# Performance work log

Hardware: AMD Instinct MI355X
Metric: run time of the kernel (lower is better)

Reference implementation:

```python
import jax, jax.numpy as jnp
import numpy as np

N = 50000   # num nodes (learners)
M = 1000    # num scenes (columns of init)
D = 256     # embedding_dim
E = 800000  # edges per meta-path graph


def _glorot(k, shape):
    fan = float(sum(shape)) if len(shape) > 1 else float(shape[0])
    return jax.random.normal(k, shape, dtype=jnp.float32) * (2.0 / fan) ** 0.5


def setup_inputs() -> dict:
    key = jax.random.key(0)
    ks = jax.random.split(key, 16)
    inp = {
        'init': jax.random.uniform(ks[0], (N, M), dtype=jnp.float32),
        'edge_index_scs': jax.random.randint(ks[1], (2, E), 0, N, dtype=jnp.int32),
        'edge_attr_scs': jax.random.uniform(ks[2], (E,), dtype=jnp.float32),
        'edge_index_sls': jax.random.randint(ks[3], (2, E), 0, N, dtype=jnp.int32),
        'edge_attr_sls': jax.random.uniform(ks[4], (E,), dtype=jnp.float32),
        'proj_w1': _glorot(ks[5], (1, 16)),
        'proj_b1': jnp.zeros((16,), jnp.float32),
        'proj_w2': _glorot(ks[6], (16, D)),
        'proj_b2': jnp.zeros((D,), jnp.float32),
    }
    for j, name in enumerate(['scs', 'sls']):
        for l in range(3):
            inp[f'{name}_W{l+1}'] = _glorot(ks[7 + j * 3 + l], (D, D))
            inp[f'{name}_b{l+1}'] = jnp.zeros((D,), jnp.float32)
    inp['att_w'] = _glorot(ks[13], (D,))
    inp['att_b'] = jnp.zeros((), jnp.float32)
    return inp


def _gcn_layer(x, row, col, w, W, b):
    xl = x @ W                                                  # [N, D]
    deg = jax.ops.segment_sum(w, col, num_segments=N) + 1.0     # self-loop weight 1
    dinv = jax.lax.rsqrt(deg)
    norm = dinv[row] * w * dinv[col]                            # [E]
    agg = jax.ops.segment_sum(norm[:, None] * xl[row], col, num_segments=N)
    return agg + (dinv * dinv)[:, None] * xl + b                # self-loop term


def _gcn3(x, ei, ea, W1, b1, W2, b2, W3, b3):
    row, col = ei[0], ei[1]
    h = jax.nn.relu(_gcn_layer(x, row, col, ea, W1, b1))
    h = jax.nn.relu(_gcn_layer(h, row, col, ea, W2, b2))
    return jax.nn.relu(_gcn_layer(h, row, col, ea, W3, b3))


def _projection(init, w1, b1, w2, b2):
    # torch loop: per row, MLP over float nonzero *indices*, mean-pooled.
    # Embedding only depends on the column index -> precompute per-column embs.
    cols = jnp.arange(M, dtype=jnp.float32)[:, None]            # [M, 1]
    col_emb = jax.nn.relu(cols @ w1 + b1) @ w2 + b2             # [M, D]
    mask = (init != 0).astype(jnp.float32)                      # [N, M]
    cnt = mask.sum(axis=1)                                      # [N]
    emb = (mask @ col_emb) / jnp.maximum(cnt, 1.0)[:, None]
    return jnp.where((cnt > 0)[:, None], emb, 0.0)


def reference(init, edge_index_scs, edge_attr_scs, edge_index_sls, edge_attr_sls,
              proj_w1, proj_b1, proj_w2, proj_b2,
              scs_W1, scs_b1, scs_W2, scs_b2, scs_W3, scs_b3,
              sls_W1, sls_b1, sls_W2, sls_b2, sls_W3, sls_b3,
              att_w, att_b):
    emb0 = _projection(init, proj_w1, proj_b1, proj_w2, proj_b2)
    out_scs = _gcn3(emb0, edge_index_scs, edge_attr_scs, scs_W1, scs_b1, scs_W2, scs_b2, scs_W3, scs_b3)
    out_sls = _gcn3(emb0, edge_index_sls, edge_attr_sls, sls_W1, sls_b1, sls_W2, sls_b2, sls_W3, sls_b3)
    emb = jnp.stack([out_scs, out_sls], axis=0)                 # [2, N, D]
    scores = jnp.einsum('pnd,d->pn', emb, att_w) + att_b        # [2, N]
    attw = jax.nn.softmax(scores, axis=0)                       # softmax over paths
    return jnp.einsum('pn,pnd->nd', attw, emb)                  # [N, D]
```

## Files before the change

kernel.cpp:

```cpp
#include <hip/hip_runtime.h>

#define N_NODES 50000
#define M_SCENE 1000
#define DIM 256
#define N_EDGES 800000
#define CAP 64
#define NBUCK 196
#define NPAD (NBUCK * 256)
#define BCAP 5120
#define ECHUNK 4096
#define SMAX 64
#define QBM 64
#define QBK 64
#define QTILES 782

typedef __attribute__((ext_vector_type(8))) short short8;
typedef __attribute__((ext_vector_type(8))) unsigned short ushort8v;
typedef __attribute__((ext_vector_type(4))) float floatx4;

__device__ __forceinline__ float bf2f(unsigned short u) {
    union { unsigned int i; float f; } v; v.i = ((unsigned int)u) << 16; return v.f;
}
__device__ __forceinline__ unsigned short f2bf(float f) {
    union { float f; unsigned int i; } v; v.f = f;
    unsigned int r = (v.i + 0x7FFFu + ((v.i >> 16) & 1u)) >> 16;
    return (unsigned short)r;
}

__device__ __forceinline__ int pinv(int k) {
    return (k & ~63) + ((k & 15) << 2) + ((k >> 4) & 3);
}

__global__ void k_col_emb(const float* __restrict__ w1, const float* __restrict__ b1,
                          const float* __restrict__ w2, const float* __restrict__ b2,
                          float* __restrict__ col_emb) {
    int m = blockIdx.x;
    int d = threadIdx.x;
    float acc = b2[d];
#pragma unroll
    for (int h = 0; h < 16; ++h) {
        float r = fmaf((float)m, w1[h], b1[h]);
        r = fmaxf(r, 0.f);
        acc = fmaf(r, w2[h * DIM + d], acc);
    }
    col_emb[m * DIM + d] = acc;
}

__global__ void k_setup(const float* __restrict__ col_emb, float* __restrict__ colsum,
                        unsigned short* __restrict__ vbf, int* __restrict__ bfill,
                        int* __restrict__ nspec) {
    int d = threadIdx.x;
    float s = 0.f;
    for (int m = 0; m < M_SCENE; ++m) s += col_emb[m * DIM + d];
    colsum[d] = s;
    vbf[d] = f2bf(s * (1.0f / (float)M_SCENE));
    for (int i = d; i < 2 * NBUCK; i += 256) bfill[i] = 0;
    if (d == 0) *nspec = 0;
}

__global__ __launch_bounds__(256) void k_scan(const float* __restrict__ init,
                                              int* __restrict__ nspec,
                                              int* __restrict__ spec_rows) {
    int row = blockIdx.x * 4 + (threadIdx.x >> 6);
    if (row >= N_NODES) return;
    int lane = threadIdx.x & 63;
    const float4* r4 = (const float4*)(init + (size_t)row * M_SCENE);
    bool z = false;
    for (int i = lane; i < 250; i += 64) {
        float4 v = r4[i];
        z |= (v.x == 0.f) | (v.y == 0.f) | (v.z == 0.f) | (v.w == 0.f);
    }
    unsigned long long mb = __ballot(z);
    if (lane == 0 && mb) {
        int p = atomicAdd(nspec, 1);
        if (p < SMAX) spec_rows[p] = row;
    }
}

__global__ __launch_bounds__(256) void k_spec(const float* __restrict__ init,
                                              const float* __restrict__ col_emb,
                                              const float* __restrict__ colsum,
                                              const int* __restrict__ nspec,
                                              const int* __restrict__ spec_rows,
                                              float* __restrict__ spec_emb) {
    int j = blockIdx.x;
    int ns = *nspec; if (ns > SMAX) ns = SMAX;
    if (j >= ns) return;
    int n = spec_rows[j];
    int t = threadIdx.x;
    __shared__ int zlist[SMAX];
    __shared__ int zcnt;
    if (t == 0) zcnt = 0;
    __syncthreads();
    const float4* row4 = (const float4*)(init + (size_t)n * M_SCENE);
    if (t < 250) {
        float4 v = row4[t];
        if (v.x == 0.f) { int p = atomicAdd(&zcnt, 1); if (p < SMAX) zlist[p] = 4 * t; }
        if (v.y == 0.f) { int p = atomicAdd(&zcnt, 1); if (p < SMAX) zlist[p] = 4 * t + 1; }
        if (v.z == 0.f) { int p = atomicAdd(&zcnt, 1); if (p < SMAX) zlist[p] = 4 * t + 2; }
        if (v.w == 0.f) { int p = atomicAdd(&zcnt, 1); if (p < SMAX) zlist[p] = 4 * t + 3; }
    }
    __syncthreads();
    int zc = zcnt; if (zc > SMAX) zc = SMAX;
    int nz = M_SCENE - zcnt;
    float s = colsum[t];
    for (int i = 0; i < zc; ++i) s -= col_emb[zlist[i] * DIM + t];
    float e = (nz > 0) ? (s / (float)nz) : 0.f;
    spec_emb[j * DIM + t] = bf2f(f2bf(e));
}

__global__ __launch_bounds__(256) void k_delta(const float* __restrict__ spec_emb,
                                               const unsigned short* __restrict__ vbf,
                                               const unsigned short* __restrict__ Wt,
                                               const int* __restrict__ nspec,
                                               float* __restrict__ delta) {
    int j = blockIdx.x, g = blockIdx.y;
    int ns = *nspec; if (ns > SMAX) ns = SMAX;
    if (j < SMAX && j >= ns) return;
    int d = threadIdx.x;
    const unsigned short* W = Wt + (size_t)(g * 3 + 0) * DIM * DIM + (size_t)d * DIM;
    float acc = 0.f;
    if (j == SMAX) {
        for (int k = 0; k < DIM; ++k) acc = fmaf(bf2f(vbf[k]), bf2f(W[k]), acc);
    } else {
        const float* x = spec_emb + j * DIM;
        for (int k = 0; k < DIM; ++k) acc = fmaf(x[k], bf2f(W[k]), acc);
    }
    delta[((size_t)g * (SMAX + 1) + j) * DIM + d] = acc;
}

__global__ __launch_bounds__(256) void k_prep_w(const float* W0, const float* W1, const float* W2,
                                                const float* W3, const float* W4, const float* W5,
                                                unsigned short* __restrict__ Wt) {
    const float* Ws[6] = {W0, W1, W2, W3, W4, W5};
    int L = blockIdx.z;
    const float* W = Ws[L];
    unsigned short* T = Wt + (size_t)L * DIM * DIM;
    bool perm = (L % 3) != 0;
    __shared__ float tile[32][33];
    int k0 = blockIdx.y * 32, n0 = blockIdx.x * 32;
    int tx = threadIdx.x & 31, ty = threadIdx.x >> 5;
    for (int r = ty; r < 32; r += 8) tile[r][tx] = W[(k0 + r) * DIM + n0 + tx];
    __syncthreads();
    int k = k0 + tx;
    int p = perm ? pinv(k) : k;
    for (int r = ty; r < 32; r += 8) T[(size_t)(n0 + r) * DIM + p] = f2bf(tile[tx][r]);
}

__global__ __launch_bounds__(256) void k_bucket(const int* __restrict__ ei0,
                                                const float* __restrict__ ea0,
                                                const int* __restrict__ ei1,
                                                const float* __restrict__ ea1,
                                                int* __restrict__ bfill,
                                                unsigned long long* __restrict__ bdata) {
    int g = blockIdx.y;
    const int* ei = g ? ei1 : ei0;
    const float* ea = g ? ea1 : ea0;
    __shared__ int hist[NBUCK];
    __shared__ int base[NBUCK];
    int t = threadIdx.x;
    for (int i = t; i < NBUCK; i += 256) hist[i] = 0;
    __syncthreads();
    int e0 = blockIdx.x * ECHUNK;
#pragma unroll
    for (int k = 0; k < ECHUNK / 256; ++k) {
        int e = e0 + k * 256 + t;
        if (e < N_EDGES) atomicAdd(&hist[ei[N_EDGES + e] >> 8], 1);
    }
    __syncthreads();
    for (int i = t; i < NBUCK; i += 256) {
        int h = hist[i];
        base[i] = h ? atomicAdd(&bfill[g * NBUCK + i], h) : 0;
        hist[i] = 0;
    }
    __syncthreads();
#pragma unroll
    for (int k = 0; k < ECHUNK / 256; ++k) {
        int e = e0 + k * 256 + t;
        if (e < N_EDGES) {
            int r = ei[e], c = ei[N_EDGES + e];
            float a = ea[e];
            int b = c >> 8;
            int off = atomicAdd(&hist[b], 1) + base[b];
            if (off < BCAP)
                bdata[((size_t)g * NBUCK + b) * BCAP + off] =
                    ((unsigned long long)(c & 255) << 32) |
                    ((unsigned long long)((unsigned int)r << 16) | f2bf(a));
        }
    }
}

__global__ __launch_bounds__(256) void k_csr(const int* __restrict__ bfill,
                                             const unsigned long long* __restrict__ bdata,
                                             int* __restrict__ cnt,
                                             unsigned int* __restrict__ slots,
                                             float* __restrict__ dinv) {
    int g = blockIdx.y, b = blockIdx.x;
    int t = threadIdx.x;
    __shared__ unsigned int lslots[256 * CAP];
    __shared__ int lcnt[256];
    lcnt[t] = 0;
    __syncthreads();
    int n = bfill[g * NBUCK + b]; if (n > BCAP) n = BCAP;
    const unsigned long long* src = bdata + ((size_t)g * NBUCK + b) * BCAP;
    for (int i = t; i < n; i += 256) {
        unsigned long long p = src[i];
        int lc = (int)(p >> 32);
        int pos = atomicAdd(&lcnt[lc], 1);
        if (pos < CAP) lslots[lc * CAP + pos] = (unsigned int)p;
    }
    __syncthreads();
    int node = b * 256 + t;
    if (node < N_NODES) {
        int c = lcnt[t]; if (c > CAP) c = CAP;
        cnt[g * N_NODES + node] = c;
        float a = 0.f;
        for (int i = 0; i < c; ++i)
            a += bf2f((unsigned short)(lslots[t * CAP + i] & 0xFFFFu));
        dinv[g * N_NODES + node] = rsqrtf(1.0f + a);
    }
    unsigned int* dst = slots + ((size_t)g * NPAD + b * 256) * CAP;
    for (int i = t; i < 256 * CAP; i += 256) dst[i] = lslots[i];
}

__global__ __launch_bounds__(256) void k_layer1(const float* __restrict__ dinv,
                                                const int* __restrict__ cnt,
                                                const unsigned int* __restrict__ slots,
                                                const int* __restrict__ nspec_p,
                                                const int* __restrict__ spec_rows,
                                                const float* __restrict__ delta,
                                                const float* __restrict__ bias0,
                                                const float* __restrict__ bias1,
                                                unsigned short* __restrict__ outp) {
    int ng = blockIdx.x * 4 + (threadIdx.x >> 6);
    if (ng >= 2 * N_NODES) return;
    int lane = threadIdx.x & 63;
    int g = ng >= N_NODES;
    int gbase = g ? N_NODES : 0;
    int n = ng - gbase;
    const float* bias = g ? bias1 : bias0;
    int c = cnt[ng];
    float dn = dinv[ng];
    int ns = *nspec_p; if (ns > SMAX) ns = SMAX;
    size_t sbase = ((size_t)g * NPAD + n) * CAP;
    float w = 0.f;
    int match = -1;
    if (lane < c) {
        unsigned int sl = slots[sbase + lane];
        int s = (int)(sl >> 16);
        w = dinv[gbase + s] * bf2f((unsigned short)(sl & 0xFFFFu)) * dn;
        for (int k = 0; k < ns; ++k)
            if (spec_rows[k] == s) { match = k; break; }
    }
    float alpha = w;
#pragma unroll
    for (int off = 32; off; off >>= 1) alpha += __shfl_xor(alpha, off, 64);
    alpha += dn * dn;
    int pc0 = ((lane >> 4) << 6) + (lane & 15);
    const float* dbase = delta + (size_t)g * (SMAX + 1) * DIM;
    const float* vwp = dbase + SMAX * DIM;
    float vw0 = vwp[pc0], vw1 = vwp[pc0 + 16], vw2 = vwp[pc0 + 32], vw3 = vwp[pc0 + 48];
    float c0 = 0.f, c1 = 0.f, c2 = 0.f, c3 = 0.f;
    unsigned long long mb = __ballot(match >= 0);
    while (mb) {
        int l = __ffsll((unsigned long long)mb) - 1;
        mb &= mb - 1;
        float wj = __shfl(w, l, 64);
        int mj = __shfl(match, l, 64);
        const float* D = dbase + mj * DIM;
        c0 = fmaf(wj, D[pc0] - vw0, c0);
        c1 = fmaf(wj, D[pc0 + 16] - vw1, c1);
        c2 = fmaf(wj, D[pc0 + 32] - vw2, c2);
        c3 = fmaf(wj, D[pc0 + 48] - vw3, c3);
    }
    int selfm = -1;
    for (int k = 0; k < ns; ++k) if (spec_rows[k] == n) selfm = k;
    if (selfm >= 0) {
        float sw = dn * dn;
        const float* D = dbase + selfm * DIM;
        c0 = fmaf(sw, D[pc0] - vw0, c0);
        c1 = fmaf(sw, D[pc0 + 16] - vw1, c1);
        c2 = fmaf(sw, D[pc0 + 32] - vw2, c2);
        c3 = fmaf(sw, D[pc0 + 48] - vw3, c3);
    }
    ushort4 o;
    o.x = f2bf(fmaxf(fmaf(alpha, vw0, c0) + bias[pc0], 0.f));
    o.y = f2bf(fmaxf(fmaf(alpha, vw1, c1) + bias[pc0 + 16], 0.f));
    o.z = f2bf(fmaxf(fmaf(alpha, vw2, c2) + bias[pc0 + 32], 0.f));
    o.w = f2bf(fmaxf(fmaf(alpha, vw3, c3) + bias[pc0 + 48], 0.f));
    ((ushort4*)outp)[(size_t)ng * 64 + lane] = o;
}

__global__ __launch_bounds__(256) void k_gemm_q(const unsigned short* __restrict__ X0,
                                                const unsigned short* __restrict__ X1,
                                                const unsigned short* __restrict__ W0,
                                                const unsigned short* __restrict__ W1,
                                                unsigned int* __restrict__ xq,
                                                float* __restrict__ qscale) {
    __shared__ unsigned short As[2][QBM * QBK];
    __shared__ unsigned short Bs[2][DIM * QBK];
    int tid = threadIdx.x;
    int w = tid >> 6, l = tid & 63;
    int gb = blockIdx.x >= QTILES;
    int bx = blockIdx.x - (gb ? QTILES : 0);
    const unsigned short* Xb = gb ? X1 : X0;
    const unsigned short* Wt = gb ? W1 : W0;
    int row0 = bx * QBM;
    floatx4 acc[16] = {};

    int innerA = (tid & 7) * 16;
    const unsigned short* gA[2];
    int soffA[2];
#pragma unroll
    for (int i = 0; i < 2; ++i) {
        int r = i * 32 + (tid >> 3);
        int grow = row0 + r; if (grow >= N_NODES) grow = N_NODES - 1;
        gA[i] = Xb + (size_t)grow * DIM + (innerA >> 1);
        soffA[i] = r * 128 + (innerA ^ ((r & 7) << 4));
    }
    const unsigned short* gB[8];
    int soffB[8];
#pragma unroll
    for (int i = 0; i < 8; ++i) {
        int nr = i * 32 + (tid >> 3);
        gB[i] = Wt + (size_t)nr * DIM + (innerA >> 1);
        soffB[i] = nr * 128 + (innerA ^ ((nr & 7) << 4));
    }
    ushort8v pa[2], pb[8];
#pragma unroll
    for (int i = 0; i < 2; ++i) pa[i] = *(const ushort8v*)(gA[i]);
#pragma unroll
    for (int i = 0; i < 8; ++i) pb[i] = *(const ushort8v*)(gB[i]);
#pragma unroll
    for (int i = 0; i < 2; ++i) *(ushort8v*)((char*)As[0] + soffA[i]) = pa[i];
#pragma unroll
    for (int i = 0; i < 8; ++i) *(ushort8v*)((char*)Bs[0] + soffB[i]) = pb[i];
    __syncthreads();

    int cur = 0;
#pragma unroll
    for (int kt = 0; kt < DIM / QBK; ++kt) {
        if (kt < DIM / QBK - 1) {
            int koff = (kt + 1) * QBK;
#pragma unroll
            for (int i = 0; i < 2; ++i) pa[i] = *(const ushort8v*)(gA[i] + koff);
#pragma unroll
            for (int i = 0; i < 8; ++i) pb[i] = *(const ushort8v*)(gB[i] + koff);
        }
#pragma unroll
        for (int s = 0; s < 2; ++s) {
            int kb = s * 64 + (l >> 4) * 16;
            int r = w * 16 + (l & 15);
            short8 a = *(const short8*)((const char*)As[cur] + r * 128 + (kb ^ ((r & 7) << 4)));
#pragma unroll
            for (int nn = 0; nn < 16; ++nn) {
                int nr = nn * 16 + (l & 15);
                short8 b = *(const short8*)((const char*)Bs[cur] + nr * 128 + (kb ^ ((nr & 7) << 4)));
                acc[nn] = __builtin_amdgcn_mfma_f32_16x16x32_bf16(a, b, acc[nn], 0, 0, 0);
            }
        }
        if (kt < DIM / QBK - 1) {
#pragma unroll
            for (int i = 0; i < 2; ++i) *(ushort8v*)((char*)As[cur ^ 1] + soffA[i]) = pa[i];
#pragma unroll
            for (int i = 0; i < 8; ++i) *(ushort8v*)((char*)Bs[cur ^ 1] + soffB[i]) = pb[i];
            __syncthreads();
            cur ^= 1;
        }
    }
    int c = l & 15, g4 = l >> 4;
    float inv[4], sc[4];
#pragma unroll
    for (int j = 0; j < 4; ++j) {
        float m = 0.f;
#pragma unroll
        for (int nn = 0; nn < 16; ++nn) m = fmaxf(m, fabsf(acc[nn][j]));
#pragma unroll
        for (int off = 1; off < 16; off <<= 1) m = fmaxf(m, __shfl_xor(m, off, 64));
        inv[j] = (m > 0.f) ? (127.0f / m) : 0.f;
        sc[j] = m * (1.0f / 127.0f);
    }
    int rbase = row0 + w * 16 + g4 * 4;
    int gofs = gb ? N_NODES : 0;
#pragma unroll
    for (int j = 0; j < 4; ++j) {
        int grow = rbase + j;
        if (grow < N_NODES) {
            if (c == 0) qscale[gofs + grow] = sc[j];
#pragma unroll
            for (int t = 0; t < 4; ++t) {
                unsigned int q0 = (unsigned int)(int)rintf(fmaf(acc[4 * t + 0][j], inv[j], 128.f));
                unsigned int q1 = (unsigned int)(int)rintf(fmaf(acc[4 * t + 1][j], inv[j], 128.f));
                unsigned int q2 = (unsigned int)(int)rintf(fmaf(acc[4 * t + 2][j], inv[j], 128.f));
                unsigned int q3 = (unsigned int)(int)rintf(fmaf(acc[4 * t + 3][j], inv[j], 128.f));
                xq[((size_t)(gofs + grow)) * 64 + t * 16 + c] =
                    q0 | (q1 << 8) | (q2 << 16) | (q3 << 24);
            }
        }
    }
}

__device__ __forceinline__ float ub(unsigned int u, int k) {
    return (float)((u >> (8 * k)) & 0xFFu);
}

__global__ __launch_bounds__(256) void k_aggregate(const unsigned int* __restrict__ xq,
                                                   const float* __restrict__ scale,
                                                   const float* __restrict__ dinv,
                                                   const int* __restrict__ cnt,
                                                   const unsigned int* __restrict__ slots,
                                                   const float* __restrict__ bias0,
                                                   const float* __restrict__ bias1,
                                                   unsigned short* __restrict__ out) {
    int ng = blockIdx.x * 4 + (threadIdx.x >> 6);
    if (ng >= 2 * N_NODES) return;
    int lane = threadIdx.x & 63;
    int g = ng >= N_NODES;
    int gbase = g ? N_NODES : 0;
    const float* bias = g ? bias1 : bias0;
    int c = cnt[ng];
    float dn = dinv[ng];
    size_t sbase = ((size_t)g * NPAD + (ng - gbase)) * CAP;
    unsigned int packed = 0;
    float wdr = 0.f;
    if (lane < c) {
        unsigned int sl = slots[sbase + lane];
        int s = (int)(sl >> 16);
        float w = dinv[gbase + s] * bf2f((unsigned short)(sl & 0xFFFFu)) * dn;
        unsigned short h = f2bf(w * scale[gbase + s]);
        packed = (sl & 0xFFFF0000u) | (unsigned int)h;
        wdr = bf2f(h);
    }
    float wdsum = wdr;
#pragma unroll
    for (int off = 32; off; off >>= 1) wdsum += __shfl_xor(wdsum, off, 64);
    size_t gb64 = (size_t)gbase * 64;
    float a0 = 0.f, a1 = 0.f, a2 = 0.f, a3 = 0.f;
    int j = 0;
    for (; j + 7 < c; j += 8) {
        unsigned int v[8];
        float wq[8];
#pragma unroll
        for (int q = 0; q < 8; ++q) {
            unsigned int u = __shfl(packed, j + q, 64);
            wq[q] = bf2f((unsigned short)(u & 0xFFFFu));
            v[q] = xq[gb64 + (size_t)(u >> 16) * 64 + lane];
        }
#pragma unroll
        for (int q = 0; q < 8; ++q) {
            a0 = fmaf(wq[q], ub(v[q], 0), a0); a1 = fmaf(wq[q], ub(v[q], 1), a1);
            a2 = fmaf(wq[q], ub(v[q], 2), a2); a3 = fmaf(wq[q], ub(v[q], 3), a3);
        }
    }
    for (; j < c; ++j) {
        unsigned int u = __shfl(packed, j, 64);
        float w0 = bf2f((unsigned short)(u & 0xFFFFu));
        unsigned int v0 = xq[gb64 + (size_t)(u >> 16) * 64 + lane];
        a0 = fmaf(w0, ub(v0, 0), a0); a1 = fmaf(w0, ub(v0, 1), a1);
        a2 = fmaf(w0, ub(v0, 2), a2); a3 = fmaf(w0, ub(v0, 3), a3);
    }
    float sd = dn * dn * scale[ng];
    unsigned int us = xq[(size_t)ng * 64 + lane];
    a0 = fmaf(sd, ub(us, 0), a0); a1 = fmaf(sd, ub(us, 1), a1);
    a2 = fmaf(sd, ub(us, 2), a2); a3 = fmaf(sd, ub(us, 3), a3);
    float off128 = 128.f * (wdsum + sd);
    int pc0 = ((lane >> 4) << 6) + (lane & 15);
    ushort4 o;
    o.x = f2bf(fmaxf(a0 - off128 + bias[pc0], 0.f));
    o.y = f2bf(fmaxf(a1 - off128 + bias[pc0 + 16], 0.f));
    o.z = f2bf(fmaxf(a2 - off128 + bias[pc0 + 32], 0.f));
    o.w = f2bf(fmaxf(a3 - off128 + bias[pc0 + 48], 0.f));
    ((ushort4*)out)[(size_t)ng * 64 + lane] = o;
}

__global__ __launch_bounds__(256) void k_agg_combine(const unsigned int* __restrict__ xq,
                                                     const float* __restrict__ scale,
                                                     const float* __restrict__ dinv,
                                                     const int* __restrict__ cnt,
                                                     const unsigned int* __restrict__ slots,
                                                     const float* __restrict__ bias0,
                                                     const float* __restrict__ bias1,
                                                     const float* __restrict__ att_w,
                                                     const float* __restrict__ att_b,
                                                     float* __restrict__ out) {
    int n = blockIdx.x * 4 + (threadIdx.x >> 6);
    if (n >= N_NODES) return;
    int lane = threadIdx.x & 63;
    int c0 = cnt[n];
    int c1 = cnt[N_NODES + n];
    float dn0 = dinv[n], dn1 = dinv[N_NODES + n];
    unsigned int p0 = 0, p1 = 0;
    float wr0 = 0.f, wr1 = 0.f;
    if (lane < c0) {
        unsigned int sl = slots[(size_t)n * CAP + lane];
        int s = (int)(sl >> 16);
        float w = dinv[s] * bf2f((unsigned short)(sl & 0xFFFFu)) * dn0;
        unsigned short h = f2bf(w * scale[s]);
        p0 = (sl & 0xFFFF0000u) | (unsigned int)h;
        wr0 = bf2f(h);
    }
    if (lane < c1) {
        unsigned int sl = slots[((size_t)NPAD + n) * CAP + lane];
        int s = (int)(sl >> 16);
        float w = dinv[N_NODES + s] * bf2f((unsigned short)(sl & 0xFFFFu)) * dn1;
        unsigned short h = f2bf(w * scale[N_NODES + s]);
        p1 = (sl & 0xFFFF0000u) | (unsigned int)h;
        wr1 = bf2f(h);
    }
    float ws0 = wr0, ws1 = wr1;
#pragma unroll
    for (int off = 32; off; off >>= 1) {
        ws0 += __shfl_xor(ws0, off, 64);
        ws1 += __shfl_xor(ws1, off, 64);
    }
    size_t g1 = (size_t)N_NODES * 64;
    float A0 = 0.f, A1 = 0.f, A2 = 0.f, A3 = 0.f;
    float B0 = 0.f, B1 = 0.f, B2 = 0.f, B3 = 0.f;
    int j = 0;
    for (; j + 7 < c0; j += 8) {
        unsigned int v[8]; float wq[8];
#pragma unroll
        for (int q = 0; q < 8; ++q) {
            unsigned int u = __shfl(p0, j + q, 64);
            wq[q] = bf2f((unsigned short)(u & 0xFFFFu));
            v[q] = xq[(size_t)(u >> 16) * 64 + lane];
        }
#pragma unroll
        for (int q = 0; q < 8; ++q) {
            A0 = fmaf(wq[q], ub(v[q], 0), A0); A1 = fmaf(wq[q], ub(v[q], 1), A1);
            A2 = fmaf(wq[q], ub(v[q], 2), A2); A3 = fmaf(wq[q], ub(v[q], 3), A3);
        }
    }
    for (; j < c0; ++j) {
        unsigned int u = __shfl(p0, j, 64);
        float w0 = bf2f((unsigned short)(u & 0xFFFFu));
        unsigned int v0 = xq[(size_t)(u >> 16) * 64 + lane];
        A0 = fmaf(w0, ub(v0, 0), A0); A1 = fmaf(w0, ub(v0, 1), A1);
        A2 = fmaf(w0, ub(v0, 2), A2); A3 = fmaf(w0, ub(v0, 3), A3);
    }
    j = 0;
    for (; j + 7 < c1; j += 8) {
        unsigned int v[8]; float wq[8];
#pragma unroll
        for (int q = 0; q < 8; ++q) {
            unsigned int u = __shfl(p1, j + q, 64);
            wq[q] = bf2f((unsigned short)(u & 0xFFFFu));
            v[q] = xq[g1 + (size_t)(u >> 16) * 64 + lane];
        }
#pragma unroll
        for (int q = 0; q < 8; ++q) {
            B0 = fmaf(wq[q], ub(v[q], 0), B0); B1 = fmaf(wq[q], ub(v[q], 1), B1);
            B2 = fmaf(wq[q], ub(v[q], 2), B2); B3 = fmaf(wq[q], ub(v[q], 3), B3);
        }
    }
    for (; j < c1; ++j) {
        unsigned int u = __shfl(p1, j, 64);
        float w0 = bf2f((unsigned short)(u & 0xFFFFu));
        unsigned int v0 = xq[g1 + (size_t)(u >> 16) * 64 + lane];
        B0 = fmaf(w0, ub(v0, 0), B0); B1 = fmaf(w0, ub(v0, 1), B1);
        B2 = fmaf(w0, ub(v0, 2), B2); B3 = fmaf(w0, ub(v0, 3), B3);
    }
    float sd0 = dn0 * dn0 * scale[n];
    float sd1 = dn1 * dn1 * scale[N_NODES + n];
    unsigned int us0 = xq[(size_t)n * 64 + lane];
    unsigned int us1 = xq[g1 + (size_t)n * 64 + lane];
    A0 = fmaf(sd0, ub(us0, 0), A0); A1 = fmaf(sd0, ub(us0, 1), A1);
    A2 = fmaf(sd0, ub(us0, 2), A2); A3 = fmaf(sd0, ub(us0, 3), A3);
    B0 = fmaf(sd1, ub(us1, 0), B0); B1 = fmaf(sd1, ub(us1, 1), B1);
    B2 = fmaf(sd1, ub(us1, 2), B2); B3 = fmaf(sd1, ub(us1, 3), B3);
    float offA = 128.f * (ws0 + sd0);
    float offB = 128.f * (ws1 + sd1);
    int pc0 = ((lane >> 4) << 6) + (lane & 15);
    float va0 = fmaxf(A0 - offA + bias0[pc0], 0.f);
    float va1 = fmaxf(A1 - offA + bias0[pc0 + 16], 0.f);
    float va2 = fmaxf(A2 - offA + bias0[pc0 + 32], 0.f);
    float va3 = fmaxf(A3 - offA + bias0[pc0 + 48], 0.f);
    float vb0 = fmaxf(B0 - offB + bias1[pc0], 0.f);
    float vb1 = fmaxf(B1 - offB + bias1[pc0 + 16], 0.f);
    float vb2 = fmaxf(B2 - offB + bias1[pc0 + 32], 0.f);
    float vb3 = fmaxf(B3 - offB + bias1[pc0 + 48], 0.f);
    float pa = va0 * att_w[pc0] + va1 * att_w[pc0 + 16]
             + va2 * att_w[pc0 + 32] + va3 * att_w[pc0 + 48];
    float pb = vb0 * att_w[pc0] + vb1 * att_w[pc0 + 16]
             + vb2 * att_w[pc0 + 32] + vb3 * att_w[pc0 + 48];
#pragma unroll
    for (int off = 32; off > 0; off >>= 1) {
        pa += __shfl_xor(pa, off, 64);
        pb += __shfl_xor(pb, off, 64);
    }
    float bbias = att_b[0];
    float sa = pa + bbias, sb = pb + bbias;
    float mx = fmaxf(sa, sb);
    float ea = __expf(sa - mx), eb = __expf(sb - mx);
    float inv = 1.f / (ea + eb);
    float wa = ea * inv, wb = eb * inv;
    float* orow = out + (size_t)n * DIM;
    orow[pc0]      = wa * va0 + wb * vb0;
    orow[pc0 + 16] = wa * va1 + wb * vb1;
    orow[pc0 + 32] = wa * va2 + wb * vb2;
    orow[pc0 + 48] = wa * va3 + wb * vb3;
}

static inline size_t align256(size_t x) { return (x + 255) & ~(size_t)255; }

extern "C" void kernel_launch(void* const* d_in, const int* in_sizes, int n_in,
                              void* d_out, int out_size, void* d_ws, size_t ws_size,
                              hipStream_t stream) {
    const float* init  = (const float*)d_in[0];
    const int*   ei0 = (const int*)d_in[1];
    const float* ea0 = (const float*)d_in[2];
    const int*   ei1 = (const int*)d_in[3];
    const float* ea1 = (const float*)d_in[4];
    const float* pw1 = (const float*)d_in[5];
    const float* pb1 = (const float*)d_in[6];
    const float* pw2 = (const float*)d_in[7];
    const float* pb2 = (const float*)d_in[8];
    const float* W[2][3];
    const float* B[2][3];
    for (int g = 0; g < 2; ++g)
        for (int l = 0; l < 3; ++l) {
            W[g][l] = (const float*)d_in[9 + g * 6 + l * 2];
            B[g][l] = (const float*)d_in[9 + g * 6 + l * 2 + 1];
        }
    const float* att_w = (const float*)d_in[21];
    const float* att_b = (const float*)d_in[22];
    float* out = (float*)d_out;

    char* ws = (char*)d_ws;
    size_t NBH  = (size_t)N_NODES * DIM * sizeof(unsigned short);
    size_t NBH2 = 2 * NBH;
    unsigned short* ACTa  = (unsigned short*)ws; ws += align256(NBH2);
    unsigned short* ACTb  = (unsigned short*)ws; ws += align256(NBH2);
    unsigned int*   XQ    = (unsigned int*)ws;   ws += align256((size_t)2 * N_NODES * DIM);
    float* qscale = (float*)ws; ws += align256((size_t)2 * N_NODES * 4);
    unsigned short* Wt    = (unsigned short*)ws; ws += align256((size_t)6 * DIM * DIM * 2);
    float* colemb = (float*)ws; ws += align256((size_t)M_SCENE * DIM * 4);
    float* colsum = (float*)ws; ws += align256(DIM * 4);
    unsigned short* vbf = (unsigned short*)ws; ws += align256(DIM * 2);
    int*   nspec  = (int*)ws;   ws += align256(4);
    int*   specr  = (int*)ws;   ws += align256(SMAX * 4);
    float* specemb = (float*)ws; ws += align256((size_t)SMAX * DIM * 4);
    float* delta  = (float*)ws; ws += align256((size_t)2 * (SMAX + 1) * DIM * 4);
    float* dinv   = (float*)ws; ws += align256((size_t)2 * N_NODES * 4);
    int*   cnt    = (int*)ws;   ws += align256((size_t)2 * N_NODES * 4);
    int*   bfill  = (int*)ws;   ws += align256((size_t)2 * NBUCK * 4);
    unsigned long long* bdata = (unsigned long long*)ws;
    ws += align256((size_t)2 * NBUCK * BCAP * 8);
    unsigned int* slots = (unsigned int*)ws; ws += align256((size_t)2 * NPAD * CAP * 4);

    dim3 b256(256);
    k_prep_w<<<dim3(8, 8, 6), b256, 0, stream>>>(W[0][0], W[0][1], W[0][2],
                                                 W[1][0], W[1][1], W[1][2], Wt);
    k_col_emb<<<M_SCENE, b256, 0, stream>>>(pw1, pb1, pw2, pb2, colemb);
    k_setup<<<1, b256, 0, stream>>>(colemb, colsum, vbf, bfill, nspec);
    k_scan<<<(N_NODES + 3) / 4, b256, 0, stream>>>(init, nspec, specr);
    k_spec<<<SMAX, b256, 0, stream>>>(init, colemb, colsum, nspec, specr, specemb);
    k_delta<<<dim3(SMAX + 1, 2), b256, 0, stream>>>(specemb, vbf, Wt, nspec, delta);

    k_bucket<<<dim3((N_EDGES + ECHUNK - 1) / ECHUNK, 2), b256, 0, stream>>>(
        ei0, ea0, ei1, ea1, bfill, bdata);
    k_csr<<<dim3(NBUCK, 2), b256, 0, stream>>>(bfill, bdata, cnt, slots, dinv);

    int nblkAgg = (2 * N_NODES + 3) / 4;
    k_layer1<<<nblkAgg, b256, 0, stream>>>(dinv, cnt, slots, nspec, specr, delta,
                                           B[0][0], B[1][0], ACTa);
    k_gemm_q<<<2 * QTILES, b256, 0, stream>>>(ACTa, ACTa + (size_t)N_NODES * DIM,
                                              Wt + (size_t)1 * DIM * DIM,
                                              Wt + (size_t)4 * DIM * DIM, XQ, qscale);
    k_aggregate<<<nblkAgg, b256, 0, stream>>>(XQ, qscale, dinv, cnt, slots,
                                              B[0][1], B[1][1], ACTb);
    k_gemm_q<<<2 * QTILES, b256, 0, stream>>>(ACTb, ACTb + (size_t)N_NODES * DIM,
                                              Wt + (size_t)2 * DIM * DIM,
                                              Wt + (size_t)5 * DIM * DIM, XQ, qscale);
    k_agg_combine<<<(N_NODES + 3) / 4, b256, 0, stream>>>(
        XQ, qscale, dinv, cnt, slots, B[0][2], B[1][2], att_w, att_b, out);
}
```

Measured before the change: 405.6 us.

## Merge row scan with edge bucketing and fuse spec/delta kernels

Combines the zero-row scan of init and the edge bucketing pass into one launch, using a block-index range split so the two independent workloads run concurrently. It also fuses the special-row embedding computation with the first-layer delta GEMV, keeping the row in shared memory and covering both paths in one block instead of two. This drops two kernel launches and a global intermediate buffer. In exchange the combined kernel reserves bucket shared memory even for scan blocks, and each delta block now does both paths serially.

Result: faster. 393.6 us (-3.0%).

```diff
diff --git a/kernel.cpp b/kernel.cpp
--- a/kernel.cpp
+++ b/kernel.cpp
@@ -9,6 +9,7 @@
 #define NPAD (NBUCK * 256)
 #define BCAP 5120
 #define ECHUNK 4096
+#define EBBLK 196
 #define SMAX 64
 #define QBM 64
 #define QBK 64
@@ -58,12 +59,54 @@
     if (d == 0) *nspec = 0;
 }
 
-__global__ __launch_bounds__(256) void k_scan(const float* __restrict__ init,
-                                              int* __restrict__ nspec,
-                                              int* __restrict__ spec_rows) {
-    int row = blockIdx.x * 4 + (threadIdx.x >> 6);
+__global__ __launch_bounds__(256) void k_scan_bucket(
+        const float* __restrict__ init, int* __restrict__ nspec, int* __restrict__ spec_rows,
+        const int* __restrict__ ei0, const float* __restrict__ ea0,
+        const int* __restrict__ ei1, const float* __restrict__ ea1,
+        int* __restrict__ bfill, unsigned long long* __restrict__ bdata) {
+    __shared__ int hist[NBUCK];
+    __shared__ int base[NBUCK];
+    int bx = blockIdx.x;
+    int t = threadIdx.x;
+    if (bx < 2 * EBBLK) {
+        int g = bx >= EBBLK;
+        int bb = bx - (g ? EBBLK : 0);
+        const int* ei = g ? ei1 : ei0;
+        const float* ea = g ? ea1 : ea0;
+        for (int i = t; i < NBUCK; i += 256) hist[i] = 0;
+        __syncthreads();
+        int e0 = bb * ECHUNK;
+#pragma unroll
+        for (int k = 0; k < ECHUNK / 256; ++k) {
+            int e = e0 + k * 256 + t;
+            if (e < N_EDGES) atomicAdd(&hist[ei[N_EDGES + e] >> 8], 1);
+        }
+        __syncthreads();
+        for (int i = t; i < NBUCK; i += 256) {
+            int h = hist[i];
+            base[i] = h ? atomicAdd(&bfill[g * NBUCK + i], h) : 0;
+            hist[i] = 0;
+        }
+        __syncthreads();
+#pragma unroll
+        for (int k = 0; k < ECHUNK / 256; ++k) {
+            int e = e0 + k * 256 + t;
+            if (e < N_EDGES) {
+                int r = ei[e], c = ei[N_EDGES + e];
+                float a = ea[e];
+                int b = c >> 8;
+                int off = atomicAdd(&hist[b], 1) + base[b];
+                if (off < BCAP)
+                    bdata[((size_t)g * NBUCK + b) * BCAP + off] =
+                        ((unsigned long long)(c & 255) << 32) |
+                        ((unsigned long long)((unsigned int)r << 16) | f2bf(a));
+            }
+        }
+        return;
+    }
+    int row = (bx - 2 * EBBLK) * 4 + (t >> 6);
     if (row >= N_NODES) return;
-    int lane = threadIdx.x & 63;
+    int lane = t & 63;
     const float4* r4 = (const float4*)(init + (size_t)row * M_SCENE);
     bool z = false;
     for (int i = lane; i < 250; i += 64) {
@@ -77,56 +120,51 @@
     }
 }
 
-__global__ __launch_bounds__(256) void k_spec(const float* __restrict__ init,
-                                              const float* __restrict__ col_emb,
-                                              const float* __restrict__ colsum,
-                                              const int* __restrict__ nspec,
-                                              const int* __restrict__ spec_rows,
-                                              float* __restrict__ spec_emb) {
+__global__ __launch_bounds__(256) void k_specdelta(const float* __restrict__ init,
+                                                   const float* __restrict__ col_emb,
+                                                   const float* __restrict__ colsum,
+                                                   const unsigned short* __restrict__ vbf,
+                                                   const unsigned short* __restrict__ Wt,
+                                                   const int* __restrict__ nspec,
+                                                   const int* __restrict__ spec_rows,
+                                                   float* __restrict__ delta) {
+    __shared__ float xrow[DIM];
+    __shared__ int zlist[SMAX];
+    __shared__ int zcnt;
     int j = blockIdx.x;
     int ns = *nspec; if (ns > SMAX) ns = SMAX;
-    if (j >= ns) return;
-    int n = spec_rows[j];
+    if (j < SMAX && j >= ns) return;
     int t = threadIdx.x;
-    __shared__ int zlist[SMAX];
-    __shared__ int zcnt;
-    if (t == 0) zcnt = 0;
+    if (j == SMAX) {
+        xrow[t] = bf2f(vbf[t]);
+    } else {
+        if (t == 0) zcnt = 0;
+        __syncthreads();
+        int n = spec_rows[j];
+        const float4* row4 = (const float4*)(init + (size_t)n * M_SCENE);
+        if (t < 250) {
+            float4 v = row4[t];
+            if (v.x == 0.f) { int p = atomicAdd(&zcnt, 1); if (p < SMAX) zlist[p] = 4 * t; }
+            if (v.y == 0.f) { int p = atomicAdd(&zcnt, 1); if (p < SMAX) zlist[p] = 4 * t + 1; }
+            if (v.z == 0.f) { int p = atomicAdd(&zcnt, 1); if (p < SMAX) zlist[p] = 4 * t + 2; }
+            if (v.w == 0.f) { int p = atomicAdd(&zcnt, 1); if (p < SMAX) zlist[p] = 4 * t + 3; }
+        }
+        __syncthreads();
+        int zc = zcnt; if (zc > SMAX) zc = SMAX;
+        int nz = M_SCENE - zcnt;
+        float s = colsum[t];
+        for (int i = 0; i < zc; ++i) s -= col_emb[zlist[i] * DIM + t];
+        float e = (nz > 0) ? (s / (float)nz) : 0.f;
+        xrow[t] = bf2f(f2bf(e));
+    }
     __syncthreads();
-    const float4* row4 = (const float4*)(init + (size_t)n * M_SCENE);
-    if (t < 250) {
-        float4 v = row4[t];
-        if (v.x == 0.f) { int p = atomicAdd(&zcnt, 1); if (p < SMAX) zlist[p] = 4 * t; }
-        if (v.y == 0.f) { int p = atomicAdd(&zcnt, 1); if (p < SMAX) zlist[p] = 4 * t + 1; }
-        if (v.z == 0.f) { int p = atomicAdd(&zcnt, 1); if (p < SMAX) zlist[p] = 4 * t + 2; }
-        if (v.w == 0.f) { int p = atomicAdd(&zcnt, 1); if (p < SMAX) zlist[p] = 4 * t + 3; }
-    }
-    __syncthreads();
-    int zc = zcnt; if (zc > SMAX) zc = SMAX;
-    int nz = M_SCENE - zcnt;
-    float s = colsum[t];
-    for (int i = 0; i < zc; ++i) s -= col_emb[zlist[i] * DIM + t];
-    float e = (nz > 0) ? (s / (float)nz) : 0.f;
-    spec_emb[j * DIM + t] = bf2f(f2bf(e));
-}
-
-__global__ __launch_bounds__(256) void k_delta(const float* __restrict__ spec_emb,
-                                               const unsigned short* __restrict__ vbf,
-                                               const unsigned short* __restrict__ Wt,
-                                               const int* __restrict__ nspec,
-                                               float* __restrict__ delta) {
-    int j = blockIdx.x, g = blockIdx.y;
-    int ns = *nspec; if (ns > SMAX) ns = SMAX;
-    if (j < SMAX && j >= ns) return;
-    int d = threadIdx.x;
-    const unsigned short* W = Wt + (size_t)(g * 3 + 0) * DIM * DIM + (size_t)d * DIM;
-    float acc = 0.f;
-    if (j == SMAX) {
-        for (int k = 0; k < DIM; ++k) acc = fmaf(bf2f(vbf[k]), bf2f(W[k]), acc);
-    } else {
-        const float* x = spec_emb + j * DIM;
-        for (int k = 0; k < DIM; ++k) acc = fmaf(x[k], bf2f(W[k]), acc);
-    }
-    delta[((size_t)g * (SMAX + 1) + j) * DIM + d] = acc;
+#pragma unroll
+    for (int g = 0; g < 2; ++g) {
+        const unsigned short* W = Wt + (size_t)(g * 3) * DIM * DIM + (size_t)t * DIM;
+        float acc = 0.f;
+        for (int k = 0; k < DIM; ++k) acc = fmaf(xrow[k], bf2f(W[k]), acc);
+        delta[((size_t)g * (SMAX + 1) + j) * DIM + t] = acc;
+    }
 }
 
 __global__ __launch_bounds__(256) void k_prep_w(const float* W0, const float* W1, const float* W2,
@@ -145,49 +183,6 @@
     int k = k0 + tx;
     int p = perm ? pinv(k) : k;
     for (int r = ty; r < 32; r += 8) T[(size_t)(n0 + r) * DIM + p] = f2bf(tile[tx][r]);
-}
-
-__global__ __launch_bounds__(256) void k_bucket(const int* __restrict__ ei0,
-                                                const float* __restrict__ ea0,
-                                                const int* __restrict__ ei1,
-                                                const float* __restrict__ ea1,
-                                                int* __restrict__ bfill,
-                                                unsigned long long* __restrict__ bdata) {
-    int g = blockIdx.y;
-    const int* ei = g ? ei1 : ei0;
-    const float* ea = g ? ea1 : ea0;
-    __shared__ int hist[NBUCK];
-    __shared__ int base[NBUCK];
-    int t = threadIdx.x;
-    for (int i = t; i < NBUCK; i += 256) hist[i] = 0;
-    __syncthreads();
-    int e0 = blockIdx.x * ECHUNK;
-#pragma unroll
-    for (int k = 0; k < ECHUNK / 256; ++k) {
-        int e = e0 + k * 256 + t;
-        if (e < N_EDGES) atomicAdd(&hist[ei[N_EDGES + e] >> 8], 1);
-    }
-    __syncthreads();
-    for (int i = t; i < NBUCK; i += 256) {
-        int h = hist[i];
-        base[i] = h ? atomicAdd(&bfill[g * NBUCK + i], h) : 0;
-        hist[i] = 0;
-    }
-    __syncthreads();
-#pragma unroll
-    for (int k = 0; k < ECHUNK / 256; ++k) {
-        int e = e0 + k * 256 + t;
-        if (e < N_EDGES) {
-            int r = ei[e], c = ei[N_EDGES + e];
-            float a = ea[e];
-            int b = c >> 8;
-            int off = atomicAdd(&hist[b], 1) + base[b];
-            if (off < BCAP)
-                bdata[((size_t)g * NBUCK + b) * BCAP + off] =
-                    ((unsigned long long)(c & 255) << 32) |
-                    ((unsigned long long)((unsigned int)r << 16) | f2bf(a));
-        }
-    }
 }
 
 __global__ __launch_bounds__(256) void k_csr(const int* __restrict__ bfill,
@@ -639,7 +634,6 @@
     unsigned short* vbf = (unsigned short*)ws; ws += align256(DIM * 2);
     int*   nspec  = (int*)ws;   ws += align256(4);
     int*   specr  = (int*)ws;   ws += align256(SMAX * 4);
-    float* specemb = (float*)ws; ws += align256((size_t)SMAX * DIM * 4);
     float* delta  = (float*)ws; ws += align256((size_t)2 * (SMAX + 1) * DIM * 4);
     float* dinv   = (float*)ws; ws += align256((size_t)2 * N_NODES * 4);
     int*   cnt    = (int*)ws;   ws += align256((size_t)2 * N_NODES * 4);
@@ -653,13 +647,11 @@
                                                  W[1][0], W[1][1], W[1][2], Wt);
     k_col_emb<<<M_SCENE, b256, 0, stream>>>(pw1, pb1, pw2, pb2, colemb);
     k_setup<<<1, b256, 0, stream>>>(colemb, colsum, vbf, bfill, nspec);
-    k_scan<<<(N_NODES + 3) / 4, b256, 0, stream>>>(init, nspec, specr);
-    k_spec<<<SMAX, b256, 0, stream>>>(init, colemb, colsum, nspec, specr, specemb);
-    k_delta<<<dim3(SMAX + 1, 2), b256, 0, stream>>>(specemb, vbf, Wt, nspec, delta);
-
-    k_bucket<<<dim3((N_EDGES + ECHUNK - 1) / ECHUNK, 2), b256, 0, stream>>>(
-        ei0, ea0, ei1, ea1, bfill, bdata);
+    k_scan_bucket<<<2 * EBBLK + (N_NODES + 3) / 4, b256, 0, stream>>>(
+        init, nspec, specr, ei0, ea0, ei1, ea1, bfill, bdata);
     k_csr<<<dim3(NBUCK, 2), b256, 0, stream>>>(bfill, bdata, cnt, slots, dinv);
+    k_specdelta<<<SMAX + 1, b256, 0, stream>>>(init, colemb, colsum, vbf, Wt,
+                                               nspec, specr, delta);
 
     int nblkAgg = (2 * N_NODES + 3) / 4;
     k_layer1<<<nblkAgg, b256, 0, stream>>>(dinv, cnt, slots, nspec, specr, delta,
```
